# Performance work log

Measured on AMD Instinct MI355X. Metric: run time of the kernel, lower is better.

Reference implementation:

```python
import jax, jax.numpy as jnp
import numpy as np

GRID = 8
NMS_SIZE = 4.0      # config['nms']: square box side length per keypoint
IOU_T = 0.1         # box_nms default iou threshold
DET_THRESH = 0.015  # config['det_thresh']
TOPK = 300          # config['topk'] (keep_top_k)
MAXC = 1024         # fixed candidate cap for jit-compatible NMS
DN = ('NCHW', 'OIHW', 'NCHW')
# (cin, cout, ksize) for 8 backbone convs + detector head convPa(3x3) + convPb(1x1)
CH = [(1,64,3),(64,64,3),(64,64,3),(64,64,3),(64,128,3),(128,128,3),(128,128,3),(128,128,3),(128,256,3),(256,65,1)]


def setup_inputs() -> dict:
    key = jax.random.key(0)
    d = {"x": jax.random.normal(jax.random.fold_in(key, 0), (8, 1, 240, 320), jnp.float32)}
    for i, (ci, co, k) in enumerate(CH):
        d[f"w{i}"] = jax.random.normal(jax.random.fold_in(key, 100 + i), (co, ci, k, k), jnp.float32) / np.float32(np.sqrt(ci * k * k))
        d[f"b{i}"] = jax.random.normal(jax.random.fold_in(key, 200 + i), (co,), jnp.float32) * 0.05
    return d


def _conv(x, w, b, relu=True):
    # 3x3 (pad 1) or 1x1 conv + bias (BN folded into scale/bias at inference) + ReLU
    y = jax.lax.conv_general_dilated(x, w, (1, 1), 'SAME', dimension_numbers=DN)
    y = y + b[None, :, None, None]
    return jax.nn.relu(y) if relu else y


def _pool(x):  # 2x2 max pool, stride 2
    return jax.lax.reduce_window(x, -jnp.inf, jax.lax.max, (1, 1, 2, 2), (1, 1, 2, 2), 'VALID')


def _box_nms(p):
    # p: (H, W) keypoint heatmap. Equal-size square boxes centered on pixels.
    H, W = p.shape
    vals, idx = jax.lax.top_k(p.reshape(-1), MAXC)          # sorted descending
    ys = (idx // W).astype(jnp.float32)
    xs = (idx % W).astype(jnp.float32)
    # IoU of equal axis-aligned squares of side NMS_SIZE
    ih = jnp.maximum(NMS_SIZE - jnp.abs(ys[:, None] - ys[None, :]), 0.0)
    iw = jnp.maximum(NMS_SIZE - jnp.abs(xs[:, None] - xs[None, :]), 0.0)
    inter = ih * iw
    iou = inter / (2.0 * NMS_SIZE * NMS_SIZE - inter)
    sup_mat = iou > IOU_T
    valid = vals > DET_THRESH
    ar = jnp.arange(MAXC)

    def body(i, keep):  # greedy NMS: box i (if kept) suppresses lower-scoring overlaps
        sup = sup_mat[i] & (ar > i) & keep[i]
        return keep & (~sup)

    keep = jax.lax.fori_loop(0, MAXC, body, valid)
    keep = keep & (jnp.cumsum(keep) <= TOPK)                # keep_top_k (scores sorted)
    out = jnp.zeros(H * W, p.dtype).at[idx].set(jnp.where(keep, vals, 0.0))
    return out.reshape(H, W)


def _forward(x, ws, bs):
    h = x
    h = _conv(h, ws[0], bs[0]); h = _conv(h, ws[1], bs[1]); h = _pool(h)
    h = _conv(h, ws[2], bs[2]); h = _conv(h, ws[3], bs[3]); h = _pool(h)
    h = _conv(h, ws[4], bs[4]); h = _conv(h, ws[5], bs[5]); h = _pool(h)
    h = _conv(h, ws[6], bs[6]); h = _conv(h, ws[7], bs[7])   # (N,128,H/8,W/8)
    a = _conv(h, ws[8], bs[8])                               # convPa -> (N,256,Hc,Wc)
    semi = _conv(a, ws[9], bs[9], relu=False)                # convPb -> (N,65,Hc,Wc)
    probc = jax.nn.softmax(semi, axis=1)[:, :-1]             # drop dustbin -> (N,64,Hc,Wc)
    N, _, Hc, Wc = probc.shape
    # pixel_shuffle(grid=8): (N,64,Hc,Wc) -> (N,Hc*8,Wc*8)
    prob = probc.reshape(N, GRID, GRID, Hc, Wc).transpose(0, 3, 1, 4, 2).reshape(N, Hc * GRID, Wc * GRID)
    prob_nms = jax.vmap(_box_nms)(prob)
    # torch returns prob[prob>=thresh] (ragged); jit-safe masked equivalent:
    pred = jnp.where(prob_nms >= DET_THRESH, prob_nms, 0.0)
    return prob, prob_nms, pred


def reference(x, w0, b0, w1, b1, w2, b2, w3, b3, w4, b4, w5, b5, w6, b6, w7, b7, w8, b8, w9, b9):
    ws = [w0, w1, w2, w3, w4, w5, w6, w7, w8, w9]
    bs = [b0, b1, b2, b3, b4, b5, b6, b7, b8, b9]
    return _forward(x, ws, bs)
```

## Files before the change

kernel.cpp:

```cpp
#include <hip/hip_runtime.h>
#include <stdint.h>

#define DET_THRESH 0.015f

#define FMA16(ACC, AV) do { \
  ACC[0]  = fmaf(AV, q0.x, ACC[0]);  ACC[1]  = fmaf(AV, q0.y, ACC[1]);  \
  ACC[2]  = fmaf(AV, q0.z, ACC[2]);  ACC[3]  = fmaf(AV, q0.w, ACC[3]);  \
  ACC[4]  = fmaf(AV, q1.x, ACC[4]);  ACC[5]  = fmaf(AV, q1.y, ACC[5]);  \
  ACC[6]  = fmaf(AV, q1.z, ACC[6]);  ACC[7]  = fmaf(AV, q1.w, ACC[7]);  \
  ACC[8]  = fmaf(AV, q2.x, ACC[8]);  ACC[9]  = fmaf(AV, q2.y, ACC[9]);  \
  ACC[10] = fmaf(AV, q2.z, ACC[10]); ACC[11] = fmaf(AV, q2.w, ACC[11]); \
  ACC[12] = fmaf(AV, q3.x, ACC[12]); ACC[13] = fmaf(AV, q3.y, ACC[13]); \
  ACC[14] = fmaf(AV, q3.z, ACC[14]); ACC[15] = fmaf(AV, q3.w, ACC[15]); } while (0)

#define FMA32(ACC, AV) do { \
  FMA16(ACC, AV); \
  ACC[16] = fmaf(AV, q4.x, ACC[16]); ACC[17] = fmaf(AV, q4.y, ACC[17]); \
  ACC[18] = fmaf(AV, q4.z, ACC[18]); ACC[19] = fmaf(AV, q4.w, ACC[19]); \
  ACC[20] = fmaf(AV, q5.x, ACC[20]); ACC[21] = fmaf(AV, q5.y, ACC[21]); \
  ACC[22] = fmaf(AV, q5.z, ACC[22]); ACC[23] = fmaf(AV, q5.w, ACC[23]); \
  ACC[24] = fmaf(AV, q6.x, ACC[24]); ACC[25] = fmaf(AV, q6.y, ACC[25]); \
  ACC[26] = fmaf(AV, q6.z, ACC[26]); ACC[27] = fmaf(AV, q6.w, ACC[27]); \
  ACC[28] = fmaf(AV, q7.x, ACC[28]); ACC[29] = fmaf(AV, q7.y, ACC[29]); \
  ACC[30] = fmaf(AV, q7.z, ACC[30]); ACC[31] = fmaf(AV, q7.w, ACC[31]); } while (0)

struct TP {
  const float* src[8];
  float* dst[8];
  int cin[8];
  int cout[8];
};

__global__ __launch_bounds__(256) void k_wT(TP tp) {
  int l = blockIdx.y;
  int n = tp.cin[l] * tp.cout[l] * 9;
  int k = blockIdx.x * 256 + threadIdx.x;
  if (k >= n) return;
  int ci9 = tp.cin[l] * 9;
  int co = k / ci9;
  int r = k - co * ci9;
  tp.dst[l][(size_t)r * tp.cout[l] + co] = tp.src[l][k];
}

template <int TW, int TH, bool POOL>
__global__ __launch_bounds__(256) void k_conv(
    const float* __restrict__ in, const float* __restrict__ wT, const float* __restrict__ bias,
    float* __restrict__ out, int CIN, int COUT, int H, int W, int tilesX)
{
  constexpr int SR = TH + 2;
  constexpr int SC = TW + 2;
  constexpr int LC = TW + 4;
  constexpr int TOTAL = 4 * SR * SC;
  __shared__ float ain[4][SR][LC];

  int tile = blockIdx.x;
  int tx = tile % tilesX, ty = tile / tilesX;
  int x0 = tx * TW, y0 = ty * TH;
  int cob = blockIdx.y * 16;
  int n = blockIdx.z;

  int tid = threadIdx.x;
  int r, c;
  if (TW == 32) { r = tid >> 5; c = tid & 31; }
  else          { r = tid / TW; c = tid - r * TW; }
  bool live = (TW * TH >= 256) || (tid < TW * TH);
  int rE = live ? r : 0;

  bool full = (y0 >= 1) && (y0 + TH + 1 <= H) && (x0 >= 1) && (x0 + TW + 1 <= W);
  size_t imgBase = (size_t)n * CIN * H * W;

  float acc[16];
#pragma unroll
  for (int j = 0; j < 16; j++) acc[j] = 0.f;

  int nch = CIN >> 2;
  for (int cc = 0; cc < nch; ++cc) {
    __syncthreads();
    if (full) {
      const float* src = in + imgBase + (size_t)(cc * 4) * H * W + (y0 - 1) * W + (x0 - 1);
      for (int m = tid; m < TOTAL; m += 256) {
        int ci = m / (SR * SC);
        int rem = m - ci * (SR * SC);
        int rr = rem / SC;
        int col = rem - rr * SC;
        ain[ci][rr][col] = src[(size_t)ci * H * W + rr * W + col];
      }
    } else {
      for (int m = tid; m < TOTAL; m += 256) {
        int ci = m / (SR * SC);
        int rem = m - ci * (SR * SC);
        int rr = rem / SC;
        int col = rem - rr * SC;
        int gy = y0 - 1 + rr, gx = x0 - 1 + col;
        float v = 0.f;
        if (gy >= 0 && gy < H && gx >= 0 && gx < W)
          v = in[imgBase + ((size_t)(cc * 4 + ci) * H + gy) * W + gx];
        ain[ci][rr][col] = v;
      }
    }
    __syncthreads();
#pragma unroll
    for (int ci = 0; ci < 4; ++ci) {
      float win[3][3];
#pragma unroll
      for (int dy = 0; dy < 3; dy++) {
        win[dy][0] = ain[ci][rE + dy][c];
        win[dy][1] = ain[ci][rE + dy][c + 1];
        win[dy][2] = ain[ci][rE + dy][c + 2];
      }
      const float* wp = wT + (size_t)((cc * 4 + ci) * 9) * COUT + cob;
#pragma unroll
      for (int tap = 0; tap < 9; tap++) {
        float4 q0 = *(const float4*)(wp + tap * COUT);
        float4 q1 = *(const float4*)(wp + tap * COUT + 4);
        float4 q2 = *(const float4*)(wp + tap * COUT + 8);
        float4 q3 = *(const float4*)(wp + tap * COUT + 12);
        float av = win[tap / 3][tap % 3];
        FMA16(acc, av);
      }
    }
  }

  float bvv[16];
  {
    const float4* bp = (const float4*)(bias + cob);
    *(float4*)&bvv[0] = bp[0]; *(float4*)&bvv[4] = bp[1];
    *(float4*)&bvv[8] = bp[2]; *(float4*)&bvv[12] = bp[3];
  }
  int x = x0 + c;
  int y = y0 + r;
  if (!POOL) {
    if (live && y < H && x < W) {
#pragma unroll
      for (int j = 0; j < 16; j++)
        out[(((size_t)n * COUT + cob + j) * H + y) * W + x] = fmaxf(acc[j] + bvv[j], 0.f);
    }
  } else {
    int Hp = H >> 1, Wp = W >> 1;
    int py = y >> 1, pxp = x >> 1;
    bool ok = ((r & 1) == 0) && ((c & 1) == 0) && (py < Hp) && (pxp < Wp);
#pragma unroll
    for (int j = 0; j < 16; j++) {
      float h = fmaxf(acc[j] + bvv[j], 0.f);
      float hc = fmaxf(h, __shfl_xor(h, 1, 64));
      float hv = fmaxf(hc, __shfl_xor(hc, 32, 64));
      if (ok)
        out[(((size_t)n * COUT + cob + j) * Hp + py) * Wp + pxp] = hv;
    }
  }
}

__global__ __launch_bounds__(256) void k_f01(
    const float* __restrict__ x, const float* __restrict__ w0g, const float* __restrict__ b0g,
    const float* __restrict__ wT1, const float* __restrict__ b1g, float* __restrict__ out)
{
  const int H = 240, W = 320;
  __shared__ float in_raw[12][36];
  __shared__ float a0[4][10][36];
  __shared__ float w0l[576];
  __shared__ float b0l[64];

  int tile = blockIdx.x;
  int tx = tile % 10, ty = tile / 10;
  int x0 = tx * 32, y0 = ty * 8;
  int cob = blockIdx.y * 32;
  int n = blockIdx.z;

  int tid = threadIdx.x;
  int r = tid >> 5;
  int c = tid & 31;

  bool fullT = (y0 >= 1) && (y0 + 9 <= H) && (x0 >= 1) && (x0 + 33 <= W);

  for (int k = tid; k < 576; k += 256) w0l[k] = w0g[k];
  if (tid < 64) b0l[tid] = b0g[tid];
  for (int m = tid; m < 432; m += 256) {
    int rr = m / 36, col = m - rr * 36;
    int gy = y0 - 2 + rr, gx = x0 - 2 + col;
    in_raw[rr][col] = (gy >= 0 && gy < H && gx >= 0 && gx < W)
                          ? x[(size_t)n * (H * W) + gy * W + gx] : 0.f;
  }

  float acc[32];
#pragma unroll
  for (int j = 0; j < 32; j++) acc[j] = 0.f;

  for (int cc = 0; cc < 16; ++cc) {
    __syncthreads();
    if (fullT) {
      for (int m = tid; m < 1360; m += 256) {
        int ch = m / 340;
        int rem = m - ch * 340;
        int rr = rem / 34;
        int col = rem - rr * 34;
        const float* wp = &w0l[(cc * 4 + ch) * 9];
        float s = b0l[cc * 4 + ch];
#pragma unroll
        for (int dy = 0; dy < 3; dy++)
#pragma unroll
          for (int dx = 0; dx < 3; dx++)
            s = fmaf(in_raw[rr + dy][col + dx], wp[dy * 3 + dx], s);
        a0[ch][rr][col] = fmaxf(s, 0.f);
      }
    } else {
      for (int m = tid; m < 1360; m += 256) {
        int ch = m / 340;
        int rem = m - ch * 340;
        int rr = rem / 34;
        int col = rem - rr * 34;
        int gy = y0 - 1 + rr, gx = x0 - 1 + col;
        float v = 0.f;
        if (gy >= 0 && gy < H && gx >= 0 && gx < W) {
          const float* wp = &w0l[(cc * 4 + ch) * 9];
          float s = b0l[cc * 4 + ch];
#pragma unroll
          for (int dy = 0; dy < 3; dy++)
#pragma unroll
            for (int dx = 0; dx < 3; dx++)
              s = fmaf(in_raw[rr + dy][col + dx], wp[dy * 3 + dx], s);
          v = fmaxf(s, 0.f);
        }
        a0[ch][rr][col] = v;
      }
    }
    __syncthreads();
#pragma unroll
    for (int ci = 0; ci < 4; ++ci) {
      float win[3][3];
#pragma unroll
      for (int dy = 0; dy < 3; dy++) {
        win[dy][0] = a0[ci][r + dy][c];
        win[dy][1] = a0[ci][r + dy][c + 1];
        win[dy][2] = a0[ci][r + dy][c + 2];
      }
      const float* wp = wT1 + (size_t)((cc * 4 + ci) * 9) * 64 + cob;
#pragma unroll
      for (int tap = 0; tap < 9; tap++) {
        float4 q0 = *(const float4*)(wp + tap * 64);
        float4 q1 = *(const float4*)(wp + tap * 64 + 4);
        float4 q2 = *(const float4*)(wp + tap * 64 + 8);
        float4 q3 = *(const float4*)(wp + tap * 64 + 12);
        float4 q4 = *(const float4*)(wp + tap * 64 + 16);
        float4 q5 = *(const float4*)(wp + tap * 64 + 20);
        float4 q6 = *(const float4*)(wp + tap * 64 + 24);
        float4 q7 = *(const float4*)(wp + tap * 64 + 28);
        float av = win[tap / 3][tap % 3];
        FMA32(acc, av);
      }
    }
  }

  float bvv[32];
  {
    const float4* bp = (const float4*)(b1g + cob);
#pragma unroll
    for (int g = 0; g < 8; g++) *(float4*)&bvv[4 * g] = bp[g];
  }
  int Hp = 120, Wp = 160;
  int py = (y0 + r) >> 1, pxp = (x0 + c) >> 1;
  bool ok = ((r & 1) == 0) && ((c & 1) == 0);
#pragma unroll
  for (int j = 0; j < 32; j++) {
    float h = fmaxf(acc[j] + bvv[j], 0.f);
    float hv = fmaxf(h, __shfl_xor(h, 32, 64));
    float hh = fmaxf(hv, __shfl_xor(hv, 1, 64));
    if (ok)
      out[(((size_t)n * 64 + cob + j) * Hp + py) * Wp + pxp] = hh;
  }
}

__global__ __launch_bounds__(256) void k_head(
    const float* __restrict__ act, const float* __restrict__ w9, const float* __restrict__ b9,
    float* __restrict__ prob, float* __restrict__ zbase)
{
  __shared__ float wl[256 * 68];
  int n = blockIdx.y;
  int tid = threadIdx.x;

  {
    float4* z = (float4*)zbase;
    int gid = (blockIdx.y * gridDim.x + blockIdx.x) * 256 + tid;
    for (int k = gid; k < 307200; k += 20480)
      z[k] = make_float4(0.f, 0.f, 0.f, 0.f);
  }

  for (int k = tid; k < 65 * 256; k += 256) {
    int co = k / 256, ci = k % 256;
    wl[ci * 68 + co] = w9[k];
  }
  for (int ci = tid; ci < 256; ci += 256) {
    wl[ci * 68 + 65] = 0.f; wl[ci * 68 + 66] = 0.f; wl[ci * 68 + 67] = 0.f;
  }
  __syncthreads();
  int px = blockIdx.x * 128 + (tid >> 1);
  int half = tid & 1;
  bool live = (px < 1200);
  int cbase = half * 34;
  int nreal = half ? 31 : 34;

  float accv[34];
#pragma unroll
  for (int i = 0; i < 34; i++) accv[i] = 0.f;

  if (live) {
    for (int ci = 0; ci < 256; ++ci) {
      float a = act[((size_t)n * 256 + ci) * 1200 + px];
      const float2* wp = (const float2*)&wl[ci * 68 + cbase];
#pragma unroll
      for (int g = 0; g < 17; g++) {
        float2 wv = wp[g];
        accv[g * 2 + 0] = fmaf(a, wv.x, accv[g * 2 + 0]);
        accv[g * 2 + 1] = fmaf(a, wv.y, accv[g * 2 + 1]);
      }
    }
  }
  for (int i = 0; i < 34; i++)
    if (i < nreal) accv[i] += b9[cbase + i];
  float m = -1e30f;
  for (int i = 0; i < 34; i++)
    if (i < nreal) m = fmaxf(m, accv[i]);
  m = fmaxf(m, __shfl_xor(m, 1, 64));
  float s = 0.f;
  for (int i = 0; i < 34; i++)
    if (i < nreal) { accv[i] = __expf(accv[i] - m); s += accv[i]; }
  s += __shfl_xor(s, 1, 64);
  float inv = 1.f / s;

  if (live) {
    int hc = px / 40, wc = px % 40;
    float* pb = prob + (size_t)n * 76800;
    int nw = half ? 30 : 34;
    for (int i = 0; i < nw; i++) {
      int co = cbase + i;
      pb[(hc * 8 + (co >> 3)) * 320 + wc * 8 + (co & 7)] = accv[i] * inv;
    }
  }
}

#define MAXC 1024
__global__ __launch_bounds__(1024) void k_nms(
    const float* __restrict__ prob, float* __restrict__ onms, float* __restrict__ opred)
{
  __shared__ unsigned sup[MAXC * 32];
  __shared__ unsigned long long skey[MAXC];
  __shared__ unsigned syx[MAXC];
  __shared__ unsigned hist[256];
  __shared__ unsigned vword[32];
  __shared__ unsigned sh_prefix, sh_K, sh_cG, sh_pG, sh_pE;

  int n = blockIdx.x;
  int tid = threadIdx.x;
  const float* p = prob + (size_t)n * 76800;
  float* on = onms + (size_t)n * 76800;
  float* op = opred + (size_t)n * 76800;

  if (tid == 0) { sh_prefix = 0u; sh_K = MAXC; sh_cG = 0u; sh_pG = 0u; sh_pE = 0u; }

  unsigned* h16 = sup;
  int wv = tid >> 6;
  for (int round = 0; round < 4; ++round) {
    for (int k = tid; k < 4096; k += 1024) h16[k] = 0u;
    __syncthreads();
    unsigned prefix = sh_prefix;
    int shift = 24 - 8 * round;
    unsigned maskHi = (round == 0) ? 0u : (0xFFFFFFFFu << (shift + 8));
    for (int k = tid; k < 76800; k += 1024) {
      unsigned b = __float_as_uint(p[k]);
      if ((b & maskHi) == prefix) atomicAdd(&h16[wv * 256 + ((b >> shift) & 255)], 1u);
    }
    __syncthreads();
    if (tid < 256) {
      unsigned s = 0u;
#pragma unroll
      for (int w = 0; w < 16; w++) s += h16[w * 256 + tid];
      hist[tid] = s;
    }
    __syncthreads();
    if (tid == 0) {
      unsigned K = sh_K, cum = 0u;
      int bin = 255;
      for (; bin >= 0; --bin) {
        unsigned cgt = hist[bin];
        if (cum + cgt >= K) break;
        cum += cgt;
      }
      sh_prefix = prefix | ((unsigned)bin << shift);
      sh_K = K - cum;
      sh_cG += cum;
    }
    __syncthreads();
  }
  unsigned T = sh_prefix;
  unsigned Kfill = sh_K;
  unsigned Cgt = sh_cG;

  unsigned* eq = sup;
  __syncthreads();
  for (int k = tid; k < 76800; k += 1024) {
    unsigned b = __float_as_uint(p[k]);
    if (b > T) {
      unsigned pos = atomicAdd(&sh_pG, 1u);
      skey[pos] = ((unsigned long long)b << 32) | (unsigned)(~(unsigned)k);
    } else if (b == T) {
      unsigned pos = atomicAdd(&sh_pE, 1u);
      if (pos < 2048u) eq[pos] = (unsigned)k;
    }
  }
  __syncthreads();
  unsigned cE = sh_pE;
  for (int k = tid; k < 2048; k += 1024)
    if ((unsigned)k >= cE) eq[k] = 0xFFFFFFFFu;
  __syncthreads();
  for (int k = 2; k <= 2048; k <<= 1) {
    for (int j = k >> 1; j > 0; j >>= 1) {
      int t = tid;
      int i = ((t & ~(j - 1)) << 1) | (t & (j - 1));
      int l = i | j;
      bool up = ((i & k) == 0);
      unsigned a = eq[i], b2 = eq[l];
      if (up ? (a > b2) : (a < b2)) { eq[i] = b2; eq[l] = a; }
      __syncthreads();
    }
  }
  for (int m2 = tid; m2 < (int)Kfill; m2 += 1024)
    skey[Cgt + m2] = ((unsigned long long)T << 32) | (unsigned)(~eq[m2]);
  __syncthreads();

  for (int k = 2; k <= MAXC; k <<= 1) {
    for (int j = k >> 1; j > 0; j >>= 1) {
      int i = tid;
      int l = i ^ j;
      if (l > i) {
        unsigned long long a = skey[i], b2 = skey[l];
        bool up = ((i & k) == 0);
        if (up ? (a < b2) : (a > b2)) { skey[i] = b2; skey[l] = a; }
      }
      __syncthreads();
    }
  }

  if (tid < 32) vword[tid] = 0u;
  __syncthreads();
  {
    unsigned long long key = skey[tid];
    unsigned vb = (unsigned)(key >> 32);
    float val = __uint_as_float(vb);
    unsigned id = ~(unsigned)key;
    unsigned y = id / 320u, xx = id - 320u * y;
    syx[tid] = (y << 16) | xx;
    if (val > DET_THRESH) atomicOr(&vword[tid >> 5], 1u << (tid & 31));
  }
  __syncthreads();

  {
    unsigned myyx = syx[tid];
    int ty = (int)(myyx >> 16), tx = (int)(myyx & 0xFFFFu);
    for (int w = 0; w < 32; ++w) {
      unsigned bits = 0u;
#pragma unroll 8
      for (int b2 = 0; b2 < 32; ++b2) {
        int j = w * 32 + b2;
        if (j > tid) {
          unsigned o = syx[j];
          int dy = ty - (int)(o >> 16); dy = dy < 0 ? -dy : dy;
          int dx = tx - (int)(o & 0xFFFFu); dx = dx < 0 ? -dx : dx;
          if (((dy | dx) < 4) && (dy + dx) <= 4) bits |= 1u << b2;
        }
      }
      sup[tid * 32 + w] = bits;
    }
  }
  __syncthreads();

  if (tid < 64) {
    int lw = tid;
    unsigned keepw = (lw < 32) ? vword[lw] : 0u;
    for (int i = 0; i < MAXC; ++i) {
      unsigned kword = __shfl(keepw, i >> 5, 64);
      if ((kword >> (i & 31)) & 1u) {
        if (lw < 32) keepw &= ~sup[i * 32 + lw];
      }
    }
    unsigned pc = (lw < 32) ? (unsigned)__builtin_popcount(keepw) : 0u;
    unsigned incl = pc;
    for (int d = 1; d < 32; d <<= 1) {
      unsigned t2 = __shfl_up(incl, d, 64);
      if (lw >= d) incl += t2;
    }
    unsigned excl = incl - pc;
    if (lw < 32) {
      int quota = 300 - (int)excl;
      if (quota <= 0) keepw = 0u;
      else if ((int)pc > quota) {
        while (__builtin_popcount(keepw) > quota)
          keepw &= ~(1u << (31 - __builtin_clz(keepw)));
      }
      unsigned kw = keepw;
      while (kw) {
        int b2 = __builtin_ffs((int)kw) - 1;
        kw &= kw - 1u;
        int i = lw * 32 + b2;
        unsigned long long key = skey[i];
        float v = __uint_as_float((unsigned)(key >> 32));
        unsigned id = ~(unsigned)key;
        on[id] = v;
        op[id] = v;
      }
    }
  }
}

extern "C" void kernel_launch(void* const* d_in, const int* in_sizes, int n_in,
                              void* d_out, int out_size, void* d_ws, size_t ws_size,
                              hipStream_t stream) {
  const float* x = (const float*)d_in[0];
  const float* w[10];
  const float* b[10];
  for (int i = 0; i < 10; ++i) {
    w[i] = (const float*)d_in[1 + 2 * i];
    b[i] = (const float*)d_in[2 + 2 * i];
  }
  float* A = (float*)d_ws;
  float* B = A + 9830400;
  float* prob  = (float*)d_out;
  float* onms  = prob + 614400;
  float* opred = onms + 614400;

  float* wT1 = onms;
  float* wT2 = wT1 + 36864;
  float* wT3 = wT2 + 36864;
  float* wT4 = wT3 + 36864;
  float* wT5 = wT4 + 73728;
  float* wT6 = wT5 + 147456;
  float* wT7 = wT6 + 147456;
  float* wT8 = wT7 + 147456;

  TP tp;
  tp.src[0] = w[1]; tp.dst[0] = wT1; tp.cin[0] = 64;  tp.cout[0] = 64;
  tp.src[1] = w[2]; tp.dst[1] = wT2; tp.cin[1] = 64;  tp.cout[1] = 64;
  tp.src[2] = w[3]; tp.dst[2] = wT3; tp.cin[2] = 64;  tp.cout[2] = 64;
  tp.src[3] = w[4]; tp.dst[3] = wT4; tp.cin[3] = 64;  tp.cout[3] = 128;
  tp.src[4] = w[5]; tp.dst[4] = wT5; tp.cin[4] = 128; tp.cout[4] = 128;
  tp.src[5] = w[6]; tp.dst[5] = wT6; tp.cin[5] = 128; tp.cout[5] = 128;
  tp.src[6] = w[7]; tp.dst[6] = wT7; tp.cin[6] = 128; tp.cout[6] = 128;
  tp.src[7] = w[8]; tp.dst[7] = wT8; tp.cin[7] = 128; tp.cout[7] = 256;
  k_wT<<<dim3(1152, 8), 256, 0, stream>>>(tp);

  k_f01<<<dim3(300, 2, 8), 256, 0, stream>>>(x, w[0], b[0], wT1, b[1], A);
  k_conv<32, 8, false><<<dim3(75, 4, 8), 256, 0, stream>>>(A, wT2, b[2], B, 64, 64, 120, 160, 5);
  k_conv<32, 8, true ><<<dim3(75, 4, 8), 256, 0, stream>>>(B, wT3, b[3], A, 64, 64, 120, 160, 5);
  k_conv<40, 6, false><<<dim3(20, 8, 8), 256, 0, stream>>>(A, wT4, b[4], B, 64, 128, 60, 80, 2);
  k_conv<32, 8, true ><<<dim3(24, 8, 8), 256, 0, stream>>>(B, wT5, b[5], A, 128, 128, 60, 80, 3);
  k_conv<40, 6, false><<<dim3(5, 8, 8), 256, 0, stream>>>(A, wT6, b[6], B, 128, 128, 30, 40, 1);
  k_conv<40, 6, false><<<dim3(5, 8, 8), 256, 0, stream>>>(B, wT7, b[7], A, 128, 128, 30, 40, 1);
  k_conv<40, 6, false><<<dim3(5, 16, 8), 256, 0, stream>>>(A, wT8, b[8], B, 128, 256, 30, 40, 1);
  k_head<<<dim3(10, 8), 256, 0, stream>>>(B, w[9], b[9], prob, onms);
  k_nms<<<dim3(8), 1024, 0, stream>>>(prob, onms, opred);
}
```

Baseline: 2.154 ms.

## Split-K the low-resolution 30x40 convs across four channel slices with a reduction kernel

The last three 3x3 convs at 30x40 resolution previously ran only 320-640 blocks. They now split the input channels into four partitions, giving each block a partial sum. A separate fuse kernel sums the four partials, adds bias and applies ReLU. This raises block count to fill the GPU, at the cost of writing and reading four partial slabs and two extra launches per layer.

```diff
diff --git a/kernel.cpp b/kernel.cpp
--- a/kernel.cpp
+++ b/kernel.cpp
@@ -148,6 +148,91 @@
         out[(((size_t)n * COUT + cob + j) * Hp + py) * Wp + pxp] = hv;
     }
   }
+}
+
+__global__ __launch_bounds__(256) void k_convp(
+    const float* __restrict__ in, const float* __restrict__ wT,
+    float* __restrict__ pout, int COUT)
+{
+  const int H = 30, W = 40;
+  constexpr int SR = 8, SC = 42, LC = 44;
+  constexpr int TOTAL = 4 * SR * SC;
+  __shared__ float ain[4][SR][LC];
+
+  int y0 = blockIdx.x * 6;
+  int cob = blockIdx.y * 16;
+  int z = blockIdx.z;
+  int n = z >> 2, split = z & 3;
+
+  int tid = threadIdx.x;
+  int r = tid / 40, c = tid - r * 40;
+  bool live = tid < 240;
+  int rE = live ? r : 0;
+
+  size_t imgBase = (size_t)n * 128 * 1200;
+
+  float acc[16];
+#pragma unroll
+  for (int j = 0; j < 16; j++) acc[j] = 0.f;
+
+  int cc0 = split * 8;
+  for (int cc = cc0; cc < cc0 + 8; ++cc) {
+    __syncthreads();
+    for (int m = tid; m < TOTAL; m += 256) {
+      int ci = m / (SR * SC);
+      int rem = m - ci * (SR * SC);
+      int rr = rem / SC;
+      int col = rem - rr * SC;
+      int gy = y0 - 1 + rr, gx = col - 1;
+      float v = 0.f;
+      if (gy >= 0 && gy < H && gx >= 0 && gx < W)
+        v = in[imgBase + ((size_t)(cc * 4 + ci) * H + gy) * W + gx];
+      ain[ci][rr][col] = v;
+    }
+    __syncthreads();
+#pragma unroll
+    for (int ci = 0; ci < 4; ++ci) {
+      float win[3][3];
+#pragma unroll
+      for (int dy = 0; dy < 3; dy++) {
+        win[dy][0] = ain[ci][rE + dy][c];
+        win[dy][1] = ain[ci][rE + dy][c + 1];
+        win[dy][2] = ain[ci][rE + dy][c + 2];
+      }
+      const float* wp = wT + (size_t)((cc * 4 + ci) * 9) * COUT + cob;
+#pragma unroll
+      for (int tap = 0; tap < 9; tap++) {
+        float4 q0 = *(const float4*)(wp + tap * COUT);
+        float4 q1 = *(const float4*)(wp + tap * COUT + 4);
+        float4 q2 = *(const float4*)(wp + tap * COUT + 8);
+        float4 q3 = *(const float4*)(wp + tap * COUT + 12);
+        float av = win[tap / 3][tap % 3];
+        FMA16(acc, av);
+      }
+    }
+  }
+
+  int y = y0 + r;
+  if (live && y < H) {
+    float* po = pout + (size_t)split * (8 * (size_t)COUT * 1200)
+              + ((size_t)n * COUT + cob) * 1200 + y * 40 + c;
+#pragma unroll
+    for (int j = 0; j < 16; j++)
+      po[(size_t)j * 1200] = acc[j];
+  }
+}
+
+__global__ __launch_bounds__(256) void k_fuse(
+    const float* __restrict__ pin, const float* __restrict__ bias,
+    float* __restrict__ out, int COUT)
+{
+  int idx = blockIdx.x * 256 + threadIdx.x;
+  int total = 8 * COUT * 1200;
+  if (idx >= total) return;
+  int co = (idx / 1200) % COUT;
+  size_t slab = (size_t)8 * COUT * 1200;
+  float s = pin[idx] + pin[idx + slab] + pin[idx + 2 * slab] + pin[idx + 3 * slab] + bias[co];
+  out[idx] = fmaxf(s, 0.f);
 }
 
 __global__ __launch_bounds__(256) void k_f01(
@@ -551,9 +636,16 @@
   k_conv<32, 8, true ><<<dim3(75, 4, 8), 256, 0, stream>>>(B, wT3, b[3], A, 64, 64, 120, 160, 5);
   k_conv<40, 6, false><<<dim3(20, 8, 8), 256, 0, stream>>>(A, wT4, b[4], B, 64, 128, 60, 80, 2);
   k_conv<32, 8, true ><<<dim3(24, 8, 8), 256, 0, stream>>>(B, wT5, b[5], A, 128, 128, 60, 80, 3);
-  k_conv<40, 6, false><<<dim3(5, 8, 8), 256, 0, stream>>>(A, wT6, b[6], B, 128, 128, 30, 40, 1);
-  k_conv<40, 6, false><<<dim3(5, 8, 8), 256, 0, stream>>>(B, wT7, b[7], A, 128, 128, 30, 40, 1);
-  k_conv<40, 6, false><<<dim3(5, 16, 8), 256, 0, stream>>>(A, wT8, b[8], B, 128, 256, 30, 40, 1);
-  k_head<<<dim3(10, 8), 256, 0, stream>>>(B, w[9], b[9], prob, onms);
+
+  float* C6 = B + 4915200;
+  float* C7 = A + 4915200;
+  k_convp<<<dim3(5, 8, 32), 256, 0, stream>>>(A, wT6, B, 128);
+  k_fuse<<<4800, 256, 0, stream>>>(B, b[6], C6, 128);
+  k_convp<<<dim3(5, 8, 32), 256, 0, stream>>>(C6, wT7, A, 128);
+  k_fuse<<<4800, 256, 0, stream>>>(A, b[7], C7, 128);
+  k_convp<<<dim3(5, 16, 32), 256, 0, stream>>>(C7, wT8, B, 256);
+  k_fuse<<<9600, 256, 0, stream>>>(B, b[8], A, 256);
+
+  k_head<<<dim3(10, 8), 256, 0, stream>>>(A, w[9], b[9], prob, onms);
   k_nms<<<dim3(8), 1024, 0, stream>>>(prob, onms, opred);
 }
```

Result: faster. 1.845 ms (-14.3%).
